# Optimization experiments

Measured on AMD Instinct MI355X. Metric: run time of the kernel, lower is better.

The kernel has to match this reference:

```python
import jax, jax.numpy as jnp
import numpy as np

B, N, E, F, U = 256, 240, 4338, 28, 100
NEG_SLOPE = 0.2  # PyG GATConv default negative_slope


def setup_inputs() -> dict:
    key = jax.random.key(0)
    ks = jax.random.split(key, 13)
    s = 0.05  # xavier-ish scale
    return {
        "inputs": jax.random.normal(ks[0], (B, N * F), jnp.float32),
        "state": jax.random.normal(ks[1], (B, N * U), jnp.float32),
        "edge_src": jax.random.randint(ks[2], (E,), 0, N, jnp.int32),
        "edge_dst": jax.random.randint(ks[3], (E,), 0, N, jnp.int32),
        # GATConv(U+F -> U): linear weight, attention vectors, output bias
        "Wg": jax.random.normal(ks[4], (U, U + F), jnp.float32) * s,
        "att_src": jax.random.normal(ks[5], (U,), jnp.float32) * s,
        "att_dst": jax.random.normal(ks[6], (U,), jnp.float32) * s,
        "gat_bias": jnp.zeros((U,), jnp.float32),
        # bias_1 added in _gc3 (self.biases[(100,)])
        "bias1": jnp.zeros((U,), jnp.float32),
        # GRU1: GRULinear(100, 200); GRU2: GRULinear(100, 100)
        "W_ru": jax.random.normal(ks[7], (U + F, 2 * U), jnp.float32) * s,
        "b_ru": jnp.zeros((2 * U,), jnp.float32),
        "W_c": jax.random.normal(ks[8], (U + F, U), jnp.float32) * s,
        "b_c": jnp.zeros((U,), jnp.float32),
    }


def _gat_gru(inputs, state, src, dst, Wg, att_src, att_dst, gat_bias, bias1,
             W_ru, b_ru, W_c, b_c):
    xi = inputs.reshape(B, N, F)
    xs = state.reshape(B, N, U)
    # _gc3: concat [state, inputs] -> GATConv per sample (vectorized here)
    x = jnp.concatenate([xs, xi], axis=2)                 # [B, N, U+F]
    h = jnp.einsum("bnf,cf->bnc", x, Wg)                  # [B, N, U]
    a_src = h @ att_src                                    # [B, N]
    a_dst = h @ att_dst                                    # [B, N]
    e = jax.nn.leaky_relu(a_src[:, src] + a_dst[:, dst], NEG_SLOPE)  # [B, E+N]
    eT = e.T                                               # [E+N, B]
    emax = jax.ops.segment_max(eT, dst, num_segments=N)    # [N, B]
    ex = jnp.exp(eT - emax[dst])
    denom = jax.ops.segment_sum(ex, dst, num_segments=N)   # [N, B]
    alpha = ex / denom[dst]                                # [E+N, B]
    msgs = h[:, src].transpose(1, 0, 2) * alpha[:, :, None]  # [E+N, B, U]
    agg = jax.ops.segment_sum(msgs, dst, num_segments=N)   # [N, B, U]
    gstate = agg.transpose(1, 0, 2) + gat_bias + bias1     # [B, N, U]
    st = gstate.reshape(B, N * U)
    # GRU gates (GRULinear concatenates [inputs, hidden] on feature dim)
    cat1 = jnp.concatenate([xi, gstate], axis=2).reshape(-1, U + F)
    ru = jax.nn.sigmoid((cat1 @ W_ru + b_ru).reshape(B, N, 2 * U))
    r = ru[..., :U].reshape(B, N * U)
    u = ru[..., U:].reshape(B, N * U)
    cat2 = jnp.concatenate([xi, (r * st).reshape(B, N, U)], axis=2).reshape(-1, U + F)
    c = jnp.tanh(cat2 @ W_c + b_c).reshape(B, N * U)
    return u * st + (1.0 - u) * c


def reference(inputs, state, edge_src, edge_dst, Wg, att_src, att_dst,
              gat_bias, bias1, W_ru, b_ru, W_c, b_c):
    # PyG GATConv default add_self_loops=True
    loops = jnp.arange(N, dtype=edge_src.dtype)
    src = jnp.concatenate([edge_src, loops])
    dst = jnp.concatenate([edge_dst, loops])
    return _gat_gru(inputs, state, src, dst, Wg, att_src, att_dst, gat_bias,
                    bias1, W_ru, b_ru, W_c, b_c)
```

## Files before the change

kernel.cpp:

```cpp
#include <hip/hip_runtime.h>

#define Bb 256
#define Nn 240
#define Ee 4338
#define Ff 28
#define Uu 100
#define Kk 128
#define Mrows (Bb * Nn)
#define ET (Ee + Nn)
#define AS 136

typedef __attribute__((ext_vector_type(8))) short bf16x8;
typedef __attribute__((ext_vector_type(4))) float f32x4;
typedef unsigned short u16;

__device__ __forceinline__ float bf2f(u16 u) {
  union { unsigned int i; float f; } v; v.i = ((unsigned int)u) << 16; return v.f;
}
__device__ __forceinline__ u16 f2bf(float f) {
  union { float ff; unsigned int i; } v; v.ff = f;
  unsigned int x = v.i;
  return (u16)((x + 0x7fffu + ((x >> 16) & 1u)) >> 16);
}
__device__ __forceinline__ void split4(const float4 v, ushort4& h, ushort4& l) {
  u16 h0 = f2bf(v.x), h1 = f2bf(v.y), h2 = f2bf(v.z), h3 = f2bf(v.w);
  h.x = h0; h.y = h1; h.z = h2; h.w = h3;
  l.x = f2bf(v.x - bf2f(h0)); l.y = f2bf(v.y - bf2f(h1));
  l.z = f2bf(v.z - bf2f(h2)); l.w = f2bf(v.w - bf2f(h3));
}

__global__ __launch_bounds__(256) void k_prep(
    const float* __restrict__ Wg, const float* __restrict__ Wru, const float* __restrict__ Wc,
    u16* __restrict__ wgh, u16* __restrict__ wgl,
    u16* __restrict__ wruh, u16* __restrict__ wrul,
    u16* __restrict__ wch, u16* __restrict__ wcl) {
  int gt = blockIdx.x * 256 + threadIdx.x, GS = gridDim.x * 256;
  for (int i = gt; i < 128 * Kk; i += GS) {
    int c = i >> 7, k = i & 127;
    float v = (c < Uu) ? Wg[c * Kk + k] : 0.f;
    u16 h = f2bf(v); wgh[i] = h; wgl[i] = f2bf(v - bf2f(h));
  }
  for (int i = gt; i < 256 * Kk; i += GS) {
    int n = i >> 7, kp = i & 127;
    int k = (kp < Uu) ? (kp + Ff) : (kp - Uu);
    float v = (n < 2 * Uu) ? Wru[k * (2 * Uu) + n] : 0.f;
    u16 h = f2bf(v); wruh[i] = h; wrul[i] = f2bf(v - bf2f(h));
  }
  for (int i = gt; i < 128 * Kk; i += GS) {
    int n = i >> 7, kp = i & 127;
    int k = (kp < Uu) ? (kp + Ff) : (kp - Uu);
    float v = (n < Uu) ? Wc[k * Uu + n] : 0.f;
    u16 h = f2bf(v); wch[i] = h; wcl[i] = f2bf(v - bf2f(h));
  }
}

__global__ __launch_bounds__(256) void k_csr(
    const int* __restrict__ esrc, const int* __restrict__ edst,
    int* __restrict__ coff, int* __restrict__ cslot) {
  __shared__ int cnt[256];
  __shared__ int scan[256];
  __shared__ int cur[Nn];
  int tid = threadIdx.x;
  cnt[tid] = 0;
  __syncthreads();
  for (int e = tid; e < Ee; e += 256) atomicAdd(&cnt[edst[e]], 1);
  __syncthreads();
  int x = (tid < Nn) ? (cnt[tid] + 1) : 0;
  int incl = x;
  scan[tid] = incl;
  __syncthreads();
#pragma unroll
  for (int d = 1; d < 256; d <<= 1) {
    int t = (tid >= d) ? scan[tid - d] : 0;
    __syncthreads();
    incl += t;
    scan[tid] = incl;
    __syncthreads();
  }
  int excl = incl - x;
  if (tid < Nn) { coff[tid] = excl; cur[tid] = excl; }
  if (tid == 0) coff[Nn] = scan[Nn - 1];
  __syncthreads();
  for (int e = tid; e < Ee; e += 256) {
    int d = edst[e];
    cslot[atomicAdd(&cur[d], 1)] = esrc[e];
  }
  for (int n = tid; n < Nn; n += 256) cslot[atomicAdd(&cur[n], 1)] = n;
}

__global__ __launch_bounds__(512, 4) void k_gemm1(
    const float* __restrict__ stt, const float* __restrict__ inp,
    const u16* __restrict__ wgh, const u16* __restrict__ wgl,
    const float* __restrict__ att_s, const float* __restrict__ att_d,
    float* __restrict__ h, float* __restrict__ asrc, float* __restrict__ adst) {
  __shared__ u16 ahL[32 * AS];
  __shared__ u16 alL[32 * AS];
  __shared__ float sredA[32], sredD[32];
  int tid = threadIdx.x;
  int m0 = blockIdx.x * 32;
  if (tid < 32) sredA[tid] = 0.f;
  else if (tid < 64) sredD[tid - 32] = 0.f;
  for (int j = tid; j < 32 * 32; j += 512) {
    int r = j >> 5, g = j & 31;
    float4 v = (g < 25) ? *(const float4*)(stt + (size_t)(m0 + r) * Uu + g * 4)
                        : *(const float4*)(inp + (size_t)(m0 + r) * Ff + (g - 25) * 4);
    ushort4 hh, ll;
    split4(v, hh, ll);
    *(ushort4*)(ahL + r * AS + g * 4) = hh;
    *(ushort4*)(alL + r * AS + g * 4) = ll;
  }
  __syncthreads();

  int w = tid >> 6, l = tid & 63, l15 = l & 15, q = l >> 4;
  f32x4 zero = {0.f, 0.f, 0.f, 0.f};

  int T = w;
  bf16x8 wh[4], wl[4];
#pragma unroll
  for (int s = 0; s < 4; ++s) {
    const int o = (T * 16 + l15) * Kk + s * 32 + q * 8;
    wh[s] = *(const bf16x8*)(wgh + o);
    wl[s] = *(const bf16x8*)(wgl + o);
  }
  f32x4 acc[2];
  acc[0] = zero; acc[1] = zero;
#pragma unroll
  for (int rt = 0; rt < 2; ++rt) {
#pragma unroll
    for (int s = 0; s < 4; ++s) {
      bf16x8 a = *(const bf16x8*)(ahL + (rt * 16 + l15) * AS + s * 32 + q * 8);
      bf16x8 b = *(const bf16x8*)(alL + (rt * 16 + l15) * AS + s * 32 + q * 8);
      acc[rt] = __builtin_amdgcn_mfma_f32_16x16x32_bf16(a, wh[s], acc[rt], 0, 0, 0);
      acc[rt] = __builtin_amdgcn_mfma_f32_16x16x32_bf16(b, wh[s], acc[rt], 0, 0, 0);
      acc[rt] = __builtin_amdgcn_mfma_f32_16x16x32_bf16(a, wl[s], acc[rt], 0, 0, 0);
    }
  }
  int c = T * 16 + l15;
  float av = (c < Uu) ? att_s[c] : 0.f, dv = (c < Uu) ? att_d[c] : 0.f;
#pragma unroll
  for (int rt = 0; rt < 2; ++rt) {
#pragma unroll
    for (int i = 0; i < 4; ++i) {
      float v = acc[rt][i];
      int row = rt * 16 + q * 4 + i;
      if (c < Uu) h[(size_t)(m0 + row) * Uu + c] = v;
      float va = v * av, vd = v * dv;
#pragma unroll
      for (int msk = 1; msk < 16; msk <<= 1) {
        va += __shfl_xor(va, msk, 64);
        vd += __shfl_xor(vd, msk, 64);
      }
      if (l15 == 0) {
        atomicAdd(&sredA[row], va);
        atomicAdd(&sredD[row], vd);
      }
    }
  }
  __syncthreads();
  if (tid < 32) {
    asrc[m0 + tid] = sredA[tid];
    adst[m0 + tid] = sredD[tid];
  }
}

__global__ __launch_bounds__(256) void k_attn(
    const int* __restrict__ coff, const int* __restrict__ cslot,
    const float* __restrict__ asrc, const float* __restrict__ adst,
    const float* __restrict__ h, const float* __restrict__ gbias, const float* __restrict__ b1,
    float* __restrict__ gsf) {
  int b = blockIdx.x;
  int w = threadIdx.x >> 6, lane = threadIdx.x & 63;
  int n = blockIdx.y * 4 + w;
  int o0 = coff[n], deg = coff[n + 1] - o0;
  float ad = adst[b * Nn + n];
  const float* hb = h + (size_t)b * Nn * Uu;
  int half = lane >> 5, ll = lane & 31;
  bool act = (ll < 25);

  float ax = 0.f, ay = 0.f, az = 0.f, aw = 0.f;
  float den = 0.f;
  for (int c0 = 0; c0 < deg; c0 += 64) {
    int e = c0 + lane;
    float we = 0.f; int s = 0;
    if (e < deg) {
      s = cslot[o0 + e];
      float sc = asrc[b * Nn + s] + ad;
      sc = (sc > 0.f) ? sc : 0.2f * sc;
      we = __expf(sc);
    }
    float d = we;
#pragma unroll
    for (int msk = 1; msk < 64; msk <<= 1) d += __shfl_xor(d, msk, 64);
    den += d;

    int cn = (deg - c0 < 64) ? (deg - c0) : 64;
    for (int e2 = 0; e2 < cn; e2 += 2) {
      int eh = e2 + half;
      float w2 = __shfl(we, eh, 64);
      int s2 = __shfl(s, eh, 64);
      if (act && eh < cn) {
        const float4 hv = *(const float4*)(hb + (size_t)s2 * Uu + ll * 4);
        ax += w2 * hv.x; ay += w2 * hv.y; az += w2 * hv.z; aw += w2 * hv.w;
      }
    }
  }
  ax += __shfl_xor(ax, 32, 64);
  ay += __shfl_xor(ay, 32, 64);
  az += __shfl_xor(az, 32, 64);
  aw += __shfl_xor(aw, 32, 64);
  if (lane < 25) {
    float inv = 1.f / den;
    int u0 = lane * 4;
    float4 o;
    o.x = ax * inv + gbias[u0 + 0] + b1[u0 + 0];
    o.y = ay * inv + gbias[u0 + 1] + b1[u0 + 1];
    o.z = az * inv + gbias[u0 + 2] + b1[u0 + 2];
    o.w = aw * inv + gbias[u0 + 3] + b1[u0 + 3];
    *(float4*)(gsf + ((size_t)b * Nn + n) * Uu + u0) = o;
  }
}

__global__ __launch_bounds__(512, 4) void k_gru(
    const float* __restrict__ gsf, const float* __restrict__ inp,
    const u16* __restrict__ wruh, const u16* __restrict__ wrul,
    const float* __restrict__ bru,
    const u16* __restrict__ wch, const u16* __restrict__ wcl,
    const float* __restrict__ bc,
    float* __restrict__ out) {
  __shared__ u16 ahL[32 * AS];
  __shared__ u16 alL[32 * AS];
  __shared__ u16 ugQ[32 * Uu];
  int tid = threadIdx.x;
  int m0 = blockIdx.x * 32;
  for (int j = tid; j < 32 * 32; j += 512) {
    int r = j >> 5, g = j & 31;
    float4 v = (g < 25) ? *(const float4*)(gsf + (size_t)(m0 + r) * Uu + g * 4)
                        : *(const float4*)(inp + (size_t)(m0 + r) * Ff + (g - 25) * 4);
    ushort4 hh, ll;
    split4(v, hh, ll);
    *(ushort4*)(ahL + r * AS + g * 4) = hh;
    *(ushort4*)(alL + r * AS + g * 4) = ll;
  }

  int w = tid >> 6, l = tid & 63, l15 = l & 15, q = l >> 4;
  int cw = w * 16 + l15;

  float sv[2][4];
#pragma unroll
  for (int rt = 0; rt < 2; ++rt) {
#pragma unroll
    for (int i = 0; i < 4; ++i) {
      int row = rt * 16 + q * 4 + i;
      sv[rt][i] = (cw < Uu) ? gsf[(size_t)(m0 + row) * Uu + cw] : 0.f;
    }
  }
  __syncthreads();

  f32x4 zero = {0.f, 0.f, 0.f, 0.f};
  float pr[2][4];

#pragma unroll
  for (int pass = 0; pass < 2; ++pass) {
    int T = pass * 8 + w;
    bf16x8 wh[4], wl[4];
#pragma unroll
    for (int s = 0; s < 4; ++s) {
      const int o = (T * 16 + l15) * Kk + s * 32 + q * 8;
      wh[s] = *(const bf16x8*)(wruh + o);
      wl[s] = *(const bf16x8*)(wrul + o);
    }
    f32x4 acc[2];
    acc[0] = zero; acc[1] = zero;
#pragma unroll
    for (int rt = 0; rt < 2; ++rt) {
#pragma unroll
      for (int s = 0; s < 4; ++s) {
        bf16x8 a = *(const bf16x8*)(ahL + (rt * 16 + l15) * AS + s * 32 + q * 8);
        bf16x8 b = *(const bf16x8*)(alL + (rt * 16 + l15) * AS + s * 32 + q * 8);
        acc[rt] = __builtin_amdgcn_mfma_f32_16x16x32_bf16(a, wh[s], acc[rt], 0, 0, 0);
        acc[rt] = __builtin_amdgcn_mfma_f32_16x16x32_bf16(b, wh[s], acc[rt], 0, 0, 0);
        acc[rt] = __builtin_amdgcn_mfma_f32_16x16x32_bf16(a, wl[s], acc[rt], 0, 0, 0);
      }
    }
    int c = T * 16 + l15;
    float bv = (c < 2 * Uu) ? bru[c] : 0.f;
#pragma unroll
    for (int rt = 0; rt < 2; ++rt) {
#pragma unroll
      for (int i = 0; i < 4; ++i) {
        int row = rt * 16 + q * 4 + i;
        float y = acc[rt][i] + bv;
        float g = 1.f / (1.f + __expf(-y));
        if (pass == 0 && c < Uu) pr[rt][i] = g * sv[rt][i];
        if (c >= Uu && c < 2 * Uu) {
          ugQ[row * Uu + (c - Uu)] = (u16)(g * 65535.f + 0.5f);
        }
      }
    }
  }

  __syncthreads();
#pragma unroll
  for (int rt = 0; rt < 2; ++rt) {
#pragma unroll
    for (int i = 0; i < 4; ++i) {
      int row = rt * 16 + q * 4 + i;
      if (cw < Uu) {
        float p = pr[rt][i];
        u16 hh = f2bf(p);
        ahL[row * AS + cw] = hh;
        alL[row * AS + cw] = f2bf(p - bf2f(hh));
      }
    }
  }
  __syncthreads();

  {
    int T = w;
    bf16x8 wh[4], wl[4];
#pragma unroll
    for (int s = 0; s < 4; ++s) {
      const int o = (T * 16 + l15) * Kk + s * 32 + q * 8;
      wh[s] = *(const bf16x8*)(wch + o);
      wl[s] = *(const bf16x8*)(wcl + o);
    }
    f32x4 acc[2];
    acc[0] = zero; acc[1] = zero;
#pragma unroll
    for (int rt = 0; rt < 2; ++rt) {
#pragma unroll
      for (int s = 0; s < 4; ++s) {
        bf16x8 a = *(const bf16x8*)(ahL + (rt * 16 + l15) * AS + s * 32 + q * 8);
        bf16x8 b = *(const bf16x8*)(alL + (rt * 16 + l15) * AS + s * 32 + q * 8);
        acc[rt] = __builtin_amdgcn_mfma_f32_16x16x32_bf16(a, wh[s], acc[rt], 0, 0, 0);
        acc[rt] = __builtin_amdgcn_mfma_f32_16x16x32_bf16(b, wh[s], acc[rt], 0, 0, 0);
        acc[rt] = __builtin_amdgcn_mfma_f32_16x16x32_bf16(a, wl[s], acc[rt], 0, 0, 0);
      }
    }
    int c = cw;
    float bv = (c < Uu) ? bc[c] : 0.f;
#pragma unroll
    for (int rt = 0; rt < 2; ++rt) {
#pragma unroll
      for (int i = 0; i < 4; ++i) {
        int row = rt * 16 + q * 4 + i;
        if (c < Uu) {
          float y = acc[rt][i] + bv;
          float cv = 1.f - 2.f / (__expf(2.f * y) + 1.f);
          float u = (float)ugQ[row * Uu + c] * (1.f / 65535.f);
          out[(size_t)(m0 + row) * Uu + c] = u * sv[rt][i] + (1.f - u) * cv;
        }
      }
    }
  }
}

extern "C" void kernel_launch(void* const* d_in, const int* in_sizes, int n_in,
                              void* d_out, int out_size, void* d_ws, size_t ws_size,
                              hipStream_t stream) {
  const float* inp   = (const float*)d_in[0];
  const float* stt   = (const float*)d_in[1];
  const int*   esrc  = (const int*)d_in[2];
  const int*   edst  = (const int*)d_in[3];
  const float* Wg    = (const float*)d_in[4];
  const float* att_s = (const float*)d_in[5];
  const float* att_d = (const float*)d_in[6];
  const float* gbias = (const float*)d_in[7];
  const float* b1    = (const float*)d_in[8];
  const float* Wru   = (const float*)d_in[9];
  const float* bru   = (const float*)d_in[10];
  const float* Wc    = (const float*)d_in[11];
  const float* bc    = (const float*)d_in[12];
  float* out = (float*)d_out;

  char* base = (char*)d_ws;
  size_t o = 0;
  auto alloc = [&](size_t bytes) -> void* {
    void* p = base + o;
    o = (o + bytes + 255) & ~(size_t)255;
    return p;
  };
  u16* wgh  = (u16*)alloc(128 * Kk * sizeof(u16));
  u16* wgl  = (u16*)alloc(128 * Kk * sizeof(u16));
  u16* wruh = (u16*)alloc(256 * Kk * sizeof(u16));
  u16* wrul = (u16*)alloc(256 * Kk * sizeof(u16));
  u16* wch  = (u16*)alloc(128 * Kk * sizeof(u16));
  u16* wcl  = (u16*)alloc(128 * Kk * sizeof(u16));
  int* coff  = (int*)alloc((Nn + 1) * sizeof(int));
  int* cslot = (int*)alloc(ET * sizeof(int));
  float* h    = (float*)alloc((size_t)Mrows * Uu * sizeof(float));
  float* asrc = (float*)alloc((size_t)Mrows * sizeof(float));
  float* adst = (float*)alloc((size_t)Mrows * sizeof(float));
  float* gsf  = (float*)alloc((size_t)Mrows * Uu * sizeof(float));

  k_prep<<<32, 256, 0, stream>>>(Wg, Wru, Wc, wgh, wgl, wruh, wrul, wch, wcl);
  k_csr<<<1, 256, 0, stream>>>(esrc, edst, coff, cslot);
  k_gemm1<<<Mrows / 32, 512, 0, stream>>>(stt, inp, wgh, wgl, att_s, att_d, h, asrc, adst);
  k_attn<<<dim3(Bb, 60), 256, 0, stream>>>(coff, cslot, asrc, adst, h, gbias, b1, gsf);
  k_gru<<<Mrows / 32, 512, 0, stream>>>(gsf, inp, wruh, wrul, bru, wch, wcl, bc, out);
}
```

Baseline: 237.0 us.

## Fuse GAT projection, attention and GRU into one per-sample kernel with LDS-resident h

```diff
diff --git a/kernel.cpp b/kernel.cpp
--- a/kernel.cpp
+++ b/kernel.cpp
@@ -88,267 +88,288 @@
   for (int n = tid; n < Nn; n += 256) cslot[atomicAdd(&cur[n], 1)] = n;
 }
 
-__global__ __launch_bounds__(512, 4) void k_gemm1(
+__global__ __launch_bounds__(512, 2) void k_fused(
     const float* __restrict__ stt, const float* __restrict__ inp,
     const u16* __restrict__ wgh, const u16* __restrict__ wgl,
     const float* __restrict__ att_s, const float* __restrict__ att_d,
-    float* __restrict__ h, float* __restrict__ asrc, float* __restrict__ adst) {
-  __shared__ u16 ahL[32 * AS];
-  __shared__ u16 alL[32 * AS];
-  __shared__ float sredA[32], sredD[32];
-  int tid = threadIdx.x;
-  int m0 = blockIdx.x * 32;
-  if (tid < 32) sredA[tid] = 0.f;
-  else if (tid < 64) sredD[tid - 32] = 0.f;
-  for (int j = tid; j < 32 * 32; j += 512) {
-    int r = j >> 5, g = j & 31;
-    float4 v = (g < 25) ? *(const float4*)(stt + (size_t)(m0 + r) * Uu + g * 4)
-                        : *(const float4*)(inp + (size_t)(m0 + r) * Ff + (g - 25) * 4);
-    ushort4 hh, ll;
-    split4(v, hh, ll);
-    *(ushort4*)(ahL + r * AS + g * 4) = hh;
-    *(ushort4*)(alL + r * AS + g * 4) = ll;
-  }
-  __syncthreads();
-
-  int w = tid >> 6, l = tid & 63, l15 = l & 15, q = l >> 4;
-  f32x4 zero = {0.f, 0.f, 0.f, 0.f};
-
-  int T = w;
-  bf16x8 wh[4], wl[4];
-#pragma unroll
-  for (int s = 0; s < 4; ++s) {
-    const int o = (T * 16 + l15) * Kk + s * 32 + q * 8;
-    wh[s] = *(const bf16x8*)(wgh + o);
-    wl[s] = *(const bf16x8*)(wgl + o);
-  }
-  f32x4 acc[2];
-  acc[0] = zero; acc[1] = zero;
-#pragma unroll
-  for (int rt = 0; rt < 2; ++rt) {
-#pragma unroll
-    for (int s = 0; s < 4; ++s) {
-      bf16x8 a = *(const bf16x8*)(ahL + (rt * 16 + l15) * AS + s * 32 + q * 8);
-      bf16x8 b = *(const bf16x8*)(alL + (rt * 16 + l15) * AS + s * 32 + q * 8);
-      acc[rt] = __builtin_amdgcn_mfma_f32_16x16x32_bf16(a, wh[s], acc[rt], 0, 0, 0);
-      acc[rt] = __builtin_amdgcn_mfma_f32_16x16x32_bf16(b, wh[s], acc[rt], 0, 0, 0);
-      acc[rt] = __builtin_amdgcn_mfma_f32_16x16x32_bf16(a, wl[s], acc[rt], 0, 0, 0);
-    }
-  }
-  int c = T * 16 + l15;
-  float av = (c < Uu) ? att_s[c] : 0.f, dv = (c < Uu) ? att_d[c] : 0.f;
-#pragma unroll
-  for (int rt = 0; rt < 2; ++rt) {
-#pragma unroll
-    for (int i = 0; i < 4; ++i) {
-      float v = acc[rt][i];
-      int row = rt * 16 + q * 4 + i;
-      if (c < Uu) h[(size_t)(m0 + row) * Uu + c] = v;
-      float va = v * av, vd = v * dv;
-#pragma unroll
-      for (int msk = 1; msk < 16; msk <<= 1) {
-        va += __shfl_xor(va, msk, 64);
-        vd += __shfl_xor(vd, msk, 64);
-      }
-      if (l15 == 0) {
-        atomicAdd(&sredA[row], va);
-        atomicAdd(&sredD[row], vd);
-      }
-    }
-  }
-  __syncthreads();
-  if (tid < 32) {
-    asrc[m0 + tid] = sredA[tid];
-    adst[m0 + tid] = sredD[tid];
-  }
-}
-
-__global__ __launch_bounds__(256) void k_attn(
     const int* __restrict__ coff, const int* __restrict__ cslot,
-    const float* __restrict__ asrc, const float* __restrict__ adst,
-    const float* __restrict__ h, const float* __restrict__ gbias, const float* __restrict__ b1,
-    float* __restrict__ gsf) {
-  int b = blockIdx.x;
-  int w = threadIdx.x >> 6, lane = threadIdx.x & 63;
-  int n = blockIdx.y * 4 + w;
-  int o0 = coff[n], deg = coff[n + 1] - o0;
-  float ad = adst[b * Nn + n];
-  const float* hb = h + (size_t)b * Nn * Uu;
-  int half = lane >> 5, ll = lane & 31;
-  bool act = (ll < 25);
-
-  float ax = 0.f, ay = 0.f, az = 0.f, aw = 0.f;
-  float den = 0.f;
-  for (int c0 = 0; c0 < deg; c0 += 64) {
-    int e = c0 + lane;
-    float we = 0.f; int s = 0;
-    if (e < deg) {
-      s = cslot[o0 + e];
-      float sc = asrc[b * Nn + s] + ad;
-      sc = (sc > 0.f) ? sc : 0.2f * sc;
-      we = __expf(sc);
-    }
-    float d = we;
-#pragma unroll
-    for (int msk = 1; msk < 64; msk <<= 1) d += __shfl_xor(d, msk, 64);
-    den += d;
-
-    int cn = (deg - c0 < 64) ? (deg - c0) : 64;
-    for (int e2 = 0; e2 < cn; e2 += 2) {
-      int eh = e2 + half;
-      float w2 = __shfl(we, eh, 64);
-      int s2 = __shfl(s, eh, 64);
-      if (act && eh < cn) {
-        const float4 hv = *(const float4*)(hb + (size_t)s2 * Uu + ll * 4);
-        ax += w2 * hv.x; ay += w2 * hv.y; az += w2 * hv.z; aw += w2 * hv.w;
-      }
-    }
-  }
-  ax += __shfl_xor(ax, 32, 64);
-  ay += __shfl_xor(ay, 32, 64);
-  az += __shfl_xor(az, 32, 64);
-  aw += __shfl_xor(aw, 32, 64);
-  if (lane < 25) {
-    float inv = 1.f / den;
-    int u0 = lane * 4;
-    float4 o;
-    o.x = ax * inv + gbias[u0 + 0] + b1[u0 + 0];
-    o.y = ay * inv + gbias[u0 + 1] + b1[u0 + 1];
-    o.z = az * inv + gbias[u0 + 2] + b1[u0 + 2];
-    o.w = aw * inv + gbias[u0 + 3] + b1[u0 + 3];
-    *(float4*)(gsf + ((size_t)b * Nn + n) * Uu + u0) = o;
-  }
-}
-
-__global__ __launch_bounds__(512, 4) void k_gru(
-    const float* __restrict__ gsf, const float* __restrict__ inp,
+    const float* __restrict__ gbias, const float* __restrict__ b1,
     const u16* __restrict__ wruh, const u16* __restrict__ wrul,
     const float* __restrict__ bru,
     const u16* __restrict__ wch, const u16* __restrict__ wcl,
     const float* __restrict__ bc,
     float* __restrict__ out) {
+  __shared__ float hbuf[Nn * Uu];
   __shared__ u16 ahL[32 * AS];
   __shared__ u16 alL[32 * AS];
+  __shared__ float gch[32 * Uu];
   __shared__ u16 ugQ[32 * Uu];
+  __shared__ float asrcL[Nn];
+  __shared__ float adstL[Nn];
+  __shared__ int coffL[Nn + 1];
+  __shared__ int cslotL[ET];
+
   int tid = threadIdx.x;
-  int m0 = blockIdx.x * 32;
-  for (int j = tid; j < 32 * 32; j += 512) {
-    int r = j >> 5, g = j & 31;
-    float4 v = (g < 25) ? *(const float4*)(gsf + (size_t)(m0 + r) * Uu + g * 4)
-                        : *(const float4*)(inp + (size_t)(m0 + r) * Ff + (g - 25) * 4);
-    ushort4 hh, ll;
-    split4(v, hh, ll);
-    *(ushort4*)(ahL + r * AS + g * 4) = hh;
-    *(ushort4*)(alL + r * AS + g * 4) = ll;
-  }
+  int b = blockIdx.x;
+  const size_t sbase = (size_t)b * Nn * Uu;
+  const size_t ibase = (size_t)b * Nn * Ff;
+
+  for (int i = tid; i < Nn + 1; i += 512) coffL[i] = coff[i];
+  for (int i = tid; i < ET; i += 512) cslotL[i] = cslot[i];
+  for (int i = tid; i < Nn; i += 512) { asrcL[i] = 0.f; adstL[i] = 0.f; }
 
   int w = tid >> 6, l = tid & 63, l15 = l & 15, q = l >> 4;
   int cw = w * 16 + l15;
-
-  float sv[2][4];
-#pragma unroll
-  for (int rt = 0; rt < 2; ++rt) {
-#pragma unroll
-    for (int i = 0; i < 4; ++i) {
-      int row = rt * 16 + q * 4 + i;
-      sv[rt][i] = (cw < Uu) ? gsf[(size_t)(m0 + row) * Uu + cw] : 0.f;
-    }
-  }
-  __syncthreads();
+  int llb = l & 31, half = l >> 5;
+
+  float4 gbv = {0.f, 0.f, 0.f, 0.f};
+  if (l < 25) {
+    int u0 = l * 4;
+    gbv.x = gbias[u0 + 0] + b1[u0 + 0];
+    gbv.y = gbias[u0 + 1] + b1[u0 + 1];
+    gbv.z = gbias[u0 + 2] + b1[u0 + 2];
+    gbv.w = gbias[u0 + 3] + b1[u0 + 3];
+  }
 
   f32x4 zero = {0.f, 0.f, 0.f, 0.f};
-  float pr[2][4];
-
-#pragma unroll
-  for (int pass = 0; pass < 2; ++pass) {
-    int T = pass * 8 + w;
+
+  {
     bf16x8 wh[4], wl[4];
 #pragma unroll
     for (int s = 0; s < 4; ++s) {
-      const int o = (T * 16 + l15) * Kk + s * 32 + q * 8;
-      wh[s] = *(const bf16x8*)(wruh + o);
-      wl[s] = *(const bf16x8*)(wrul + o);
-    }
-    f32x4 acc[2];
-    acc[0] = zero; acc[1] = zero;
-#pragma unroll
-    for (int rt = 0; rt < 2; ++rt) {
-#pragma unroll
-      for (int s = 0; s < 4; ++s) {
-        bf16x8 a = *(const bf16x8*)(ahL + (rt * 16 + l15) * AS + s * 32 + q * 8);
-        bf16x8 b = *(const bf16x8*)(alL + (rt * 16 + l15) * AS + s * 32 + q * 8);
-        acc[rt] = __builtin_amdgcn_mfma_f32_16x16x32_bf16(a, wh[s], acc[rt], 0, 0, 0);
-        acc[rt] = __builtin_amdgcn_mfma_f32_16x16x32_bf16(b, wh[s], acc[rt], 0, 0, 0);
-        acc[rt] = __builtin_amdgcn_mfma_f32_16x16x32_bf16(a, wl[s], acc[rt], 0, 0, 0);
-      }
-    }
-    int c = T * 16 + l15;
-    float bv = (c < 2 * Uu) ? bru[c] : 0.f;
-#pragma unroll
-    for (int rt = 0; rt < 2; ++rt) {
+      const int o = cw * Kk + s * 32 + q * 8;
+      wh[s] = *(const bf16x8*)(wgh + o);
+      wl[s] = *(const bf16x8*)(wgl + o);
+    }
+    float av = (cw < Uu) ? att_s[cw] : 0.f;
+    float dv = (cw < Uu) ? att_d[cw] : 0.f;
+
+    for (int ch0 = 0; ch0 < Nn; ch0 += 32) {
+      int rows = Nn - ch0; if (rows > 32) rows = 32;
+      int nrt = rows >> 4;
+      for (int j = tid; j < rows * 32; j += 512) {
+        int r = j >> 5, g = j & 31;
+        float4 v = (g < 25)
+            ? *(const float4*)(stt + sbase + (size_t)(ch0 + r) * Uu + g * 4)
+            : *(const float4*)(inp + ibase + (size_t)(ch0 + r) * Ff + (g - 25) * 4);
+        ushort4 hh, lo;
+        split4(v, hh, lo);
+        *(ushort4*)(ahL + r * AS + g * 4) = hh;
+        *(ushort4*)(alL + r * AS + g * 4) = lo;
+      }
+      __syncthreads();
+      f32x4 acc[2]; acc[0] = zero; acc[1] = zero;
+#pragma unroll
+      for (int rt = 0; rt < 2; ++rt) if (rt < nrt) {
+#pragma unroll
+        for (int s = 0; s < 4; ++s) {
+          bf16x8 a = *(const bf16x8*)(ahL + (rt * 16 + l15) * AS + s * 32 + q * 8);
+          bf16x8 bb = *(const bf16x8*)(alL + (rt * 16 + l15) * AS + s * 32 + q * 8);
+          acc[rt] = __builtin_amdgcn_mfma_f32_16x16x32_bf16(a, wh[s], acc[rt], 0, 0, 0);
+          acc[rt] = __builtin_amdgcn_mfma_f32_16x16x32_bf16(bb, wh[s], acc[rt], 0, 0, 0);
+          acc[rt] = __builtin_amdgcn_mfma_f32_16x16x32_bf16(a, wl[s], acc[rt], 0, 0, 0);
+        }
+      }
+#pragma unroll
+      for (int rt = 0; rt < 2; ++rt) if (rt < nrt) {
+#pragma unroll
+        for (int i = 0; i < 4; ++i) {
+          float v = acc[rt][i];
+          int row = rt * 16 + q * 4 + i;
+          if (cw < Uu) hbuf[(ch0 + row) * Uu + cw] = v;
+          float va = v * av, vd = v * dv;
+#pragma unroll
+          for (int msk = 1; msk < 16; msk <<= 1) {
+            va += __shfl_xor(va, msk, 64);
+            vd += __shfl_xor(vd, msk, 64);
+          }
+          if (l15 == 0) {
+            atomicAdd(&asrcL[ch0 + row], va);
+            atomicAdd(&adstL[ch0 + row], vd);
+          }
+        }
+      }
+      __syncthreads();
+    }
+  }
+
+  bf16x8 r0h[4], r0l[4], r1h[4], r1l[4], cch[4], ccl[4];
+  int cw1 = 128 + cw;
+#pragma unroll
+  for (int s = 0; s < 4; ++s) {
+    const int o0 = cw * Kk + s * 32 + q * 8;
+    const int o1 = cw1 * Kk + s * 32 + q * 8;
+    r0h[s] = *(const bf16x8*)(wruh + o0);
+    r0l[s] = *(const bf16x8*)(wrul + o0);
+    r1h[s] = *(const bf16x8*)(wruh + o1);
+    r1l[s] = *(const bf16x8*)(wrul + o1);
+    cch[s] = *(const bf16x8*)(wch + o0);
+    ccl[s] = *(const bf16x8*)(wcl + o0);
+  }
+  float bru0 = bru[cw];
+  float bru1 = (cw1 < 2 * Uu) ? bru[cw1] : 0.f;
+  float bcv = (cw < Uu) ? bc[cw] : 0.f;
+
+  for (int ch0 = 0; ch0 < Nn; ch0 += 32) {
+    int rows = Nn - ch0; if (rows > 32) rows = 32;
+    int nrt = rows >> 4;
+
+    for (int n = ch0 + w; n < ch0 + rows; n += 8) {
+      int o0 = coffL[n], deg = coffL[n + 1] - o0;
+      float ad = adstL[n];
+      float ax = 0.f, ay = 0.f, az = 0.f, aw2 = 0.f, den = 0.f;
+      for (int c0 = 0; c0 < deg; c0 += 64) {
+        int e = c0 + l;
+        float we = 0.f; int s = 0;
+        if (e < deg) {
+          s = cslotL[o0 + e];
+          float sc = asrcL[s] + ad;
+          sc = (sc > 0.f) ? sc : 0.2f * sc;
+          we = __expf(sc);
+        }
+        float d = we;
+#pragma unroll
+        for (int msk = 1; msk < 64; msk <<= 1) d += __shfl_xor(d, msk, 64);
+        den += d;
+        int cn = deg - c0; if (cn > 64) cn = 64;
+        for (int e2 = 0; e2 < cn; e2 += 2) {
+          int eh = e2 + half;
+          float w2 = __shfl(we, eh, 64);
+          int s2 = __shfl(s, eh, 64);
+          if ((llb < 25) && eh < cn) {
+            const float4 hv = *(const float4*)(hbuf + s2 * Uu + llb * 4);
+            ax += w2 * hv.x; ay += w2 * hv.y; az += w2 * hv.z; aw2 += w2 * hv.w;
+          }
+        }
+      }
+      ax += __shfl_xor(ax, 32, 64);
+      ay += __shfl_xor(ay, 32, 64);
+      az += __shfl_xor(az, 32, 64);
+      aw2 += __shfl_xor(aw2, 32, 64);
+      if (l < 25) {
+        float inv = 1.f / den;
+        float4 o;
+        o.x = ax * inv + gbv.x;
+        o.y = ay * inv + gbv.y;
+        o.z = az * inv + gbv.z;
+        o.w = aw2 * inv + gbv.w;
+        *(float4*)(gch + (n - ch0) * Uu + l * 4) = o;
+      }
+    }
+    __syncthreads();
+
+    for (int j = tid; j < rows * 32; j += 512) {
+      int r = j >> 5, g = j & 31;
+      float4 v = (g < 25)
+          ? *(const float4*)(gch + r * Uu + g * 4)
+          : *(const float4*)(inp + ibase + (size_t)(ch0 + r) * Ff + (g - 25) * 4);
+      ushort4 hh, lo;
+      split4(v, hh, lo);
+      *(ushort4*)(ahL + r * AS + g * 4) = hh;
+      *(ushort4*)(alL + r * AS + g * 4) = lo;
+    }
+    float sv[2][4];
+#pragma unroll
+    for (int rt = 0; rt < 2; ++rt) if (rt < nrt) {
 #pragma unroll
       for (int i = 0; i < 4; ++i) {
         int row = rt * 16 + q * 4 + i;
-        float y = acc[rt][i] + bv;
-        float g = 1.f / (1.f + __expf(-y));
-        if (pass == 0 && c < Uu) pr[rt][i] = g * sv[rt][i];
-        if (c >= Uu && c < 2 * Uu) {
-          ugQ[row * Uu + (c - Uu)] = (u16)(g * 65535.f + 0.5f);
-        }
-      }
-    }
-  }
-
-  __syncthreads();
-#pragma unroll
-  for (int rt = 0; rt < 2; ++rt) {
-#pragma unroll
-    for (int i = 0; i < 4; ++i) {
-      int row = rt * 16 + q * 4 + i;
-      if (cw < Uu) {
-        float p = pr[rt][i];
-        u16 hh = f2bf(p);
-        ahL[row * AS + cw] = hh;
-        alL[row * AS + cw] = f2bf(p - bf2f(hh));
-      }
-    }
-  }
-  __syncthreads();
-
-  {
-    int T = w;
-    bf16x8 wh[4], wl[4];
-#pragma unroll
-    for (int s = 0; s < 4; ++s) {
-      const int o = (T * 16 + l15) * Kk + s * 32 + q * 8;
-      wh[s] = *(const bf16x8*)(wch + o);
-      wl[s] = *(const bf16x8*)(wcl + o);
-    }
-    f32x4 acc[2];
-    acc[0] = zero; acc[1] = zero;
-#pragma unroll
-    for (int rt = 0; rt < 2; ++rt) {
-#pragma unroll
-      for (int s = 0; s < 4; ++s) {
-        bf16x8 a = *(const bf16x8*)(ahL + (rt * 16 + l15) * AS + s * 32 + q * 8);
-        bf16x8 b = *(const bf16x8*)(alL + (rt * 16 + l15) * AS + s * 32 + q * 8);
-        acc[rt] = __builtin_amdgcn_mfma_f32_16x16x32_bf16(a, wh[s], acc[rt], 0, 0, 0);
-        acc[rt] = __builtin_amdgcn_mfma_f32_16x16x32_bf16(b, wh[s], acc[rt], 0, 0, 0);
-        acc[rt] = __builtin_amdgcn_mfma_f32_16x16x32_bf16(a, wl[s], acc[rt], 0, 0, 0);
-      }
-    }
-    int c = cw;
-    float bv = (c < Uu) ? bc[c] : 0.f;
-#pragma unroll
-    for (int rt = 0; rt < 2; ++rt) {
+        sv[rt][i] = (cw < Uu) ? gch[row * Uu + cw] : 0.f;
+      }
+    }
+    __syncthreads();
+
+    float pr[2][4];
+    {
+      f32x4 acc[2]; acc[0] = zero; acc[1] = zero;
+#pragma unroll
+      for (int rt = 0; rt < 2; ++rt) if (rt < nrt) {
+#pragma unroll
+        for (int s = 0; s < 4; ++s) {
+          bf16x8 a = *(const bf16x8*)(ahL + (rt * 16 + l15) * AS + s * 32 + q * 8);
+          bf16x8 bb = *(const bf16x8*)(alL + (rt * 16 + l15) * AS + s * 32 + q * 8);
+          acc[rt] = __builtin_amdgcn_mfma_f32_16x16x32_bf16(a, r0h[s], acc[rt], 0, 0, 0);
+          acc[rt] = __builtin_amdgcn_mfma_f32_16x16x32_bf16(bb, r0h[s], acc[rt], 0, 0, 0);
+          acc[rt] = __builtin_amdgcn_mfma_f32_16x16x32_bf16(a, r0l[s], acc[rt], 0, 0, 0);
+        }
+      }
+#pragma unroll
+      for (int rt = 0; rt < 2; ++rt) if (rt < nrt) {
+#pragma unroll
+        for (int i = 0; i < 4; ++i) {
+          int row = rt * 16 + q * 4 + i;
+          float y = acc[rt][i] + bru0;
+          float g = 1.f / (1.f + __expf(-y));
+          if (cw < Uu) pr[rt][i] = g * sv[rt][i];
+          else ugQ[row * Uu + (cw - Uu)] = (u16)(g * 65535.f + 0.5f);
+        }
+      }
+    }
+    {
+      f32x4 acc[2]; acc[0] = zero; acc[1] = zero;
+#pragma unroll
+      for (int rt = 0; rt < 2; ++rt) if (rt < nrt) {
+#pragma unroll
+        for (int s = 0; s < 4; ++s) {
+          bf16x8 a = *(const bf16x8*)(ahL + (rt * 16 + l15) * AS + s * 32 + q * 8);
+          bf16x8 bb = *(const bf16x8*)(alL + (rt * 16 + l15) * AS + s * 32 + q * 8);
+          acc[rt] = __builtin_amdgcn_mfma_f32_16x16x32_bf16(a, r1h[s], acc[rt], 0, 0, 0);
+          acc[rt] = __builtin_amdgcn_mfma_f32_16x16x32_bf16(bb, r1h[s], acc[rt], 0, 0, 0);
+          acc[rt] = __builtin_amdgcn_mfma_f32_16x16x32_bf16(a, r1l[s], acc[rt], 0, 0, 0);
+        }
+      }
+#pragma unroll
+      for (int rt = 0; rt < 2; ++rt) if (rt < nrt) {
+#pragma unroll
+        for (int i = 0; i < 4; ++i) {
+          int row = rt * 16 + q * 4 + i;
+          float y = acc[rt][i] + bru1;
+          float g = 1.f / (1.f + __expf(-y));
+          if (cw1 < 2 * Uu) ugQ[row * Uu + (cw1 - Uu)] = (u16)(g * 65535.f + 0.5f);
+        }
+      }
+    }
+    __syncthreads();
+
+#pragma unroll
+    for (int rt = 0; rt < 2; ++rt) if (rt < nrt) {
 #pragma unroll
       for (int i = 0; i < 4; ++i) {
         int row = rt * 16 + q * 4 + i;
-        if (c < Uu) {
-          float y = acc[rt][i] + bv;
-          float cv = 1.f - 2.f / (__expf(2.f * y) + 1.f);
-          float u = (float)ugQ[row * Uu + c] * (1.f / 65535.f);
-          out[(size_t)(m0 + row) * Uu + c] = u * sv[rt][i] + (1.f - u) * cv;
+        if (cw < Uu) {
+          float p = pr[rt][i];
+          u16 hh = f2bf(p);
+          ahL[row * AS + cw] = hh;
+          alL[row * AS + cw] = f2bf(p - bf2f(hh));
+        }
+      }
+    }
+    __syncthreads();
+
+    {
+      f32x4 acc[2]; acc[0] = zero; acc[1] = zero;
+#pragma unroll
+      for (int rt = 0; rt < 2; ++rt) if (rt < nrt) {
+#pragma unroll
+        for (int s = 0; s < 4; ++s) {
+          bf16x8 a = *(const bf16x8*)(ahL + (rt * 16 + l15) * AS + s * 32 + q * 8);
+          bf16x8 bb = *(const bf16x8*)(alL + (rt * 16 + l15) * AS + s * 32 + q * 8);
+          acc[rt] = __builtin_amdgcn_mfma_f32_16x16x32_bf16(a, cch[s], acc[rt], 0, 0, 0);
+          acc[rt] = __builtin_amdgcn_mfma_f32_16x16x32_bf16(bb, cch[s], acc[rt], 0, 0, 0);
+          acc[rt] = __builtin_amdgcn_mfma_f32_16x16x32_bf16(a, ccl[s], acc[rt], 0, 0, 0);
+        }
+      }
+#pragma unroll
+      for (int rt = 0; rt < 2; ++rt) if (rt < nrt) {
+#pragma unroll
+        for (int i = 0; i < 4; ++i) {
+          int row = rt * 16 + q * 4 + i;
+          if (cw < Uu) {
+            float y = acc[rt][i] + bcv;
+            float cv = 1.f - 2.f / (__expf(2.f * y) + 1.f);
+            float u = (float)ugQ[row * Uu + cw] * (1.f / 65535.f);
+            out[sbase + (size_t)(ch0 + row) * Uu + cw] = u * sv[rt][i] + (1.f - u) * cv;
+          }
         }
       }
     }
@@ -388,14 +409,9 @@
   u16* wcl  = (u16*)alloc(128 * Kk * sizeof(u16));
   int* coff  = (int*)alloc((Nn + 1) * sizeof(int));
   int* cslot = (int*)alloc(ET * sizeof(int));
-  float* h    = (float*)alloc((size_t)Mrows * Uu * sizeof(float));
-  float* asrc = (float*)alloc((size_t)Mrows * sizeof(float));
-  float* adst = (float*)alloc((size_t)Mrows * sizeof(float));
-  float* gsf  = (float*)alloc((size_t)Mrows * Uu * sizeof(float));
 
   k_prep<<<32, 256, 0, stream>>>(Wg, Wru, Wc, wgh, wgl, wruh, wrul, wch, wcl);
   k_csr<<<1, 256, 0, stream>>>(esrc, edst, coff, cslot);
-  k_gemm1<<<Mrows / 32, 512, 0, stream>>>(stt, inp, wgh, wgl, att_s, att_d, h, asrc, adst);
-  k_attn<<<dim3(Bb, 60), 256, 0, stream>>>(coff, cslot, asrc, adst, h, gbias, b1, gsf);
-  k_gru<<<Mrows / 32, 512, 0, stream>>>(gsf, inp, wruh, wrul, bru, wch, wcl, bc, out);
-}
+  k_fused<<<Bb, 512, 0, stream>>>(stt, inp, wgh, wgl, att_s, att_d, coff, cslot,
+                                  gbias, b1, wruh, wrul, bru, wch, wcl, bc, out);
+}
```

Result: faster. 230.9 us (-2.5%).
